# Performance work log

Hardware: AMD Instinct MI355X
Metric: run time of the kernel (lower is better)

Reference implementation:

```python
import jax, jax.numpy as jnp
import numpy as np

B, CN, DEG, IN_F, OUT_F, K = 32, 1024, 2, 128, 128, 10
NODES = [1, 16, 128, 1024]


def setup_inputs() -> dict:
    key = jax.random.key(0)
    ks = jax.random.split(key, 16)
    d = {}
    for i, n in enumerate(NODES):
        d[f"tree{i}"] = jax.random.normal(ks[i], (B, n, IN_F), dtype=jnp.float32)
    for i in range(4):
        d[f"Uw{i}"] = jax.random.normal(ks[4 + i], (IN_F, OUT_F), dtype=jnp.float32) * 0.05
        d[f"Ub{i}"] = jnp.zeros((OUT_F,), dtype=jnp.float32)
    d["W_up"] = jax.random.normal(ks[8], (CN, IN_F, DEG * IN_F), dtype=jnp.float32) * 0.05
    d["Fw0"] = jax.random.normal(ks[9], (IN_F, K * IN_F), dtype=jnp.float32) * 0.05
    d["Fb0"] = jnp.zeros((K * IN_F,), dtype=jnp.float32)
    d["Fw1"] = jax.random.normal(ks[10], (K * IN_F, OUT_F), dtype=jnp.float32) * 0.05
    d["Fb1"] = jnp.zeros((OUT_F,), dtype=jnp.float32)
    d["b_bias"] = jax.random.normal(ks[11], (1, DEG * CN, OUT_F), dtype=jnp.float32) * 0.05
    return d


def reference(tree0, tree1, tree2, tree3,
              Uw0, Ub0, Uw1, Ub1, Uw2, Ub2, Uw3, Ub3,
              W_up, Fw0, Fb0, Fw1, Fb1, b_bias):
    tree = [tree0, tree1, tree2, tree3]
    Uw = [Uw0, Uw1, Uw2, Uw3]
    Ub = [Ub0, Ub1, Ub2, Ub3]
    curr_node = W_up.shape[0]
    in_feat = W_up.shape[1]
    degree = W_up.shape[2] // in_feat

    # Ancestor info: project each depth, then tile each ancestor node's
    # projected vector to cover its descendants at the current level.
    anc = jnp.zeros((tree[0].shape[0], curr_node, Uw0.shape[1]), dtype=tree0.dtype)
    for t, w, b in zip(tree, Uw, Ub):
        Q = t @ w + b                       # [B, anc_node, out_feat]
        rep = curr_node // t.shape[1]
        anc = anc + jnp.repeat(Q, rep, axis=1)  # == tf.tile([1,1,rep]) + reshape

    # Per-node unique-weight upsample: [B,n,1,in] @ [n,in,deg*in]
    nl = jnp.einsum('bni,nio->bno', tree[-1], W_up)            # [B, CN, deg*in]
    nl = nl.reshape(nl.shape[0], curr_node * degree, in_feat)   # [B, CN*deg, in]
    nl = (nl @ Fw0 + Fb0) @ Fw1 + Fb1                           # Dense chain
    nl = nl + jnp.repeat(anc, degree, axis=1)                   # broadcast ancestors
    nl = nl + b_bias
    return jnp.where(nl >= 0, nl, 0.2 * nl)                     # LeakyReLU(0.2)
```

## Files before the change

kernel.cpp:

```cpp
#include <hip/hip_runtime.h>
#include <stdint.h>


using short8   = __attribute__((ext_vector_type(8))) short;
using floatx16 = __attribute__((ext_vector_type(16))) float;

__device__ __forceinline__ unsigned short f2bf(float f) {
    unsigned int u = __builtin_bit_cast(unsigned int, f);
    return (unsigned short)((u + 0x8000u) >> 16);
}

#define FB_OFF  524288
#define FF_OFF  524416
#define UW_OFF  532608

__global__ __launch_bounds__(256) void ffused_p1(
    const float* __restrict__ Fw0, const float* __restrict__ Fb0,
    const float* __restrict__ Fw1, float* __restrict__ P)
{
    const int kc = blockIdx.x;
    const int i  = blockIdx.y;
    const int j  = threadIdx.x & 127;
    const int il = threadIdx.x >> 7;
    const int k0 = kc * 160 + il * 80;
    const float* __restrict__ src = (i < 128) ? (Fw0 + (size_t)i * 1280) : Fb0;
    float acc = 0.f;
    #pragma unroll 8
    for (int kk = 0; kk < 80; ++kk)
        acc += src[k0 + kk] * Fw1[(size_t)(k0 + kk) * 128 + j];
    P[(size_t)(kc * 2 + il) * 16512 + i * 128 + j] = acc;
}

__global__ __launch_bounds__(256) void prep2(
    const float* __restrict__ P, const float* __restrict__ Fb1,
    const float* __restrict__ Uw0, const float* __restrict__ Uw1,
    const float* __restrict__ Uw2, const float* __restrict__ Uw3,
    unsigned short* __restrict__ FfusedBF, float* __restrict__ Fbias,
    unsigned short* __restrict__ UwBF)
{
    if (blockIdx.x < 65) {
        const int idx = blockIdx.x * 256 + threadIdx.x;
        if (idx >= 16512) return;
        const int i = idx >> 7, j = idx & 127;
        float s = 0.f;
        #pragma unroll
        for (int p = 0; p < 16; ++p) s += P[(size_t)p * 16512 + idx];
        if (i < 128) FfusedBF[(((i >> 3) * 128) + j) * 8 + (i & 7)] = f2bf(s);
        else         Fbias[j] = s + Fb1[j];
    } else {
        const int bx  = blockIdx.x - 65;
        const int mat = bx >> 4;
        const int kg  = bx & 15;
        const float* __restrict__ Uw = (mat == 0) ? Uw0 : (mat == 1) ? Uw1
                                     : (mat == 2) ? Uw2 : Uw3;
        const int col = threadIdx.x & 127;
        const int kh  = threadIdx.x >> 7;
        #pragma unroll
        for (int q = 0; q < 4; ++q) {
            const int kk = kh * 4 + q;
            const float v = Uw[(size_t)(kg * 8 + kk) * 128 + col];
            UwBF[(((size_t)(mat * 16 + kg) * 128) + col) * 8 + kk] = f2bf(v);
        }
    }
}

__global__ __launch_bounds__(256, 2) void tree_main(
    const float* __restrict__ t0, const float* __restrict__ t1,
    const float* __restrict__ t2, const float* __restrict__ t3,
    const float* __restrict__ Ub0, const float* __restrict__ Ub1,
    const float* __restrict__ Ub2, const float* __restrict__ Ub3,
    const float* __restrict__ Wup, const float* __restrict__ bbias,
    const unsigned short* __restrict__ FfusedBF,
    const unsigned short* __restrict__ UwBF,
    const float* __restrict__ Fbias,
    float* __restrict__ out)
{
    const int n    = blockIdx.x;
    const int tid  = threadIdx.x;
    const int w    = tid >> 6;
    const int lane = tid & 63;
    const int l31  = lane & 31;
    const int half = lane >> 5;
    const int colq = w * 32 + l31;
    const int i2   = n >> 3;

    __shared__ __align__(16) unsigned char smem_raw[33792 + 2 * 16384];
    unsigned short* Alds = (unsigned short*)smem_raw;
    unsigned short* Ulds = (unsigned short*)smem_raw;
    float* wbuf0 = (float*)(smem_raw + 33792);
    float* wbuf1 = (float*)(smem_raw + 33792 + 16384);

    const float* __restrict__ Wtile = Wup + (size_t)n * 32768;
#define ISSUE_W(T, WB) \
    { _Pragma("unroll") \
      for (int q = 0; q < 4; ++q) { \
        const int chunk = (tid >> 6) * 4 + q; \
        const float* gp = Wtile + (T) * 4096 + chunk * 256 + (tid & 63) * 4; \
        float* lp = (WB) + chunk * 256; \
        __builtin_amdgcn_global_load_lds( \
            (const __attribute__((address_space(1))) unsigned int*)gp, \
            (__attribute__((address_space(3))) unsigned int*)lp, 16, 0, 0); \
      } }

    ISSUE_W(0, wbuf0)
    ISSUE_W(1, wbuf1)

    #pragma unroll
    for (int mi = 0; mi < 4; ++mi) {
        const float* __restrict__ base = (mi == 0) ? t0 : (mi == 1) ? t1
                                       : (mi == 2) ? t2 : t3;
        #pragma unroll
        for (int i = 0; i < 4; ++i) {
            const int idx = i * 256 + tid;
            const int b   = idx >> 5;
            const int q   = idx & 31;
            int row;
            if      (mi == 0) row = b;
            else if (mi == 1) row = b * 16 + (i2 >> 3);
            else if (mi == 2) row = b * 128 + i2;
            else              row = b * 1024 + n;
            const float4 v = *reinterpret_cast<const float4*>(
                base + (size_t)row * 128 + q * 4);
            ushort4 u;
            u.x = f2bf(v.x); u.y = f2bf(v.y); u.z = f2bf(v.z); u.w = f2bf(v.w);
            *reinterpret_cast<ushort4*>(
                &Alds[((mi * 16 + (q >> 1)) * 33 + b) * 8 + (q & 1) * 4]) = u;
        }
    }
    __syncthreads();

    floatx16 qacc, accT0, accT1;
    #pragma unroll
    for (int r = 0; r < 16; ++r) { qacc[r] = 0.f; accT0[r] = 0.f; accT1[r] = 0.f; }

    #pragma unroll
    for (int ks = 0; ks < 24; ++ks) {
        const int kg = 2 * ks + half;
        const short8 a  = *reinterpret_cast<const short8*>(&Alds[(kg * 33 + l31) * 8]);
        const short8 bf = *reinterpret_cast<const short8*>(
            &UwBF[((size_t)kg * 128 + colq) * 8]);
        qacc = __builtin_amdgcn_mfma_f32_32x32x16_bf16(a, bf, qacc, 0, 0, 0);
    }

#define WBODY_L(WT, WB) \
    { const int kg = 48 + 2 * (WT) + half; \
      const short8 a  = *reinterpret_cast<const short8*>(&Alds[(kg * 33 + l31) * 8]); \
      const short8 bf = *reinterpret_cast<const short8*>( \
          &UwBF[((size_t)kg * 128 + colq) * 8]); \
      qacc = __builtin_amdgcn_mfma_f32_32x32x16_bf16(a, bf, qacc, 0, 0, 0); \
      short8 a0, a1; \
      _Pragma("unroll") \
      for (int jj = 0; jj < 8; ++jj) { \
          a0[jj] = (short)f2bf((WB)[(half * 8 + jj) * 256 + w * 64 + l31]); \
          a1[jj] = (short)f2bf((WB)[(half * 8 + jj) * 256 + w * 64 + 32 + l31]); } \
      accT0 = __builtin_amdgcn_mfma_f32_32x32x16_bf16(a0, a, accT0, 0, 0, 0); \
      accT1 = __builtin_amdgcn_mfma_f32_32x32x16_bf16(a1, a, accT1, 0, 0, 0); }

    WBODY_L(0, wbuf0) __syncthreads(); ISSUE_W(2, wbuf0)
    WBODY_L(1, wbuf1) __syncthreads(); ISSUE_W(3, wbuf1)
    WBODY_L(2, wbuf0) __syncthreads(); ISSUE_W(4, wbuf0)
    WBODY_L(3, wbuf1) __syncthreads(); ISSUE_W(5, wbuf1)
    WBODY_L(4, wbuf0) __syncthreads(); ISSUE_W(6, wbuf0)
    WBODY_L(5, wbuf1) __syncthreads(); ISSUE_W(7, wbuf1)
    WBODY_L(6, wbuf0) __syncthreads();
    WBODY_L(7, wbuf1)

    __syncthreads();

    #pragma unroll
    for (int tt = 0; tt < 2; ++tt) {
        const floatx16 Av = tt ? accT1 : accT0;
        #pragma unroll
        for (int r = 0; r < 16; ++r) {
            const int cm = w * 64 + tt * 32 + ((r & 3) + 8 * (r >> 2) + 4 * half);
            const int d  = cm >> 7;
            const int cp = cm & 127;
            Ulds[(((cp >> 3) * 65) + d * 32 + l31) * 8 + (cp & 7)] = f2bf(Av[r]);
        }
    }
    __syncthreads();

    const float ubsum = Ub0[colq] + Ub1[colq] + Ub2[colq] + Ub3[colq] + Fbias[colq];
    const float bb0 = bbias[(size_t)(2 * n + 0) * 128 + colq];
    const float bb1 = bbias[(size_t)(2 * n + 1) * 128 + colq];

    floatx16 o0, o1;
    #pragma unroll
    for (int r = 0; r < 16; ++r) { o0[r] = 0.f; o1[r] = 0.f; }
    #pragma unroll
    for (int ks = 0; ks < 8; ++ks) {
        const int kg2 = 2 * ks + half;
        const short8 a0 = *reinterpret_cast<const short8*>(&Ulds[(kg2 * 65 + l31) * 8]);
        const short8 a1 = *reinterpret_cast<const short8*>(&Ulds[(kg2 * 65 + 32 + l31) * 8]);
        const short8 bf = *reinterpret_cast<const short8*>(
            &FfusedBF[(((size_t)kg2 * 128) + colq) * 8]);
        o0 = __builtin_amdgcn_mfma_f32_32x32x16_bf16(a0, bf, o0, 0, 0, 0);
        o1 = __builtin_amdgcn_mfma_f32_32x32x16_bf16(a1, bf, o1, 0, 0, 0);
    }

    #pragma unroll
    for (int r = 0; r < 16; ++r) {
        const int brow = (r & 3) + 8 * (r >> 2) + 4 * half;
        const float addc = qacc[r] + ubsum;
        float v0 = o0[r] + addc + bb0;
        float v1 = o1[r] + addc + bb1;
        v0 = (v0 >= 0.f) ? v0 : 0.2f * v0;
        v1 = (v1 >= 0.f) ? v1 : 0.2f * v1;
        const size_t idx0 = ((size_t)brow * 2048 + 2 * n) * 128 + colq;
        out[idx0]       = v0;
        out[idx0 + 128] = v1;
    }
}

extern "C" void kernel_launch(void* const* d_in, const int* in_sizes, int n_in,
                              void* d_out, int out_size, void* d_ws, size_t ws_size,
                              hipStream_t stream) {
    const float* t0  = (const float*)d_in[0];
    const float* t1  = (const float*)d_in[1];
    const float* t2  = (const float*)d_in[2];
    const float* t3  = (const float*)d_in[3];
    const float* Uw0 = (const float*)d_in[4];
    const float* Ub0 = (const float*)d_in[5];
    const float* Uw1 = (const float*)d_in[6];
    const float* Ub1 = (const float*)d_in[7];
    const float* Uw2 = (const float*)d_in[8];
    const float* Ub2 = (const float*)d_in[9];
    const float* Uw3 = (const float*)d_in[10];
    const float* Ub3 = (const float*)d_in[11];
    const float* Wup = (const float*)d_in[12];
    const float* Fw0 = (const float*)d_in[13];
    const float* Fb0 = (const float*)d_in[14];
    const float* Fw1 = (const float*)d_in[15];
    const float* Fb1 = (const float*)d_in[16];
    const float* bb  = (const float*)d_in[17];

    float* ws = (float*)d_ws;
    float* P              = ws;
    float* Fbias          = ws + FB_OFF;
    unsigned short* FfBF  = (unsigned short*)(ws + FF_OFF);
    unsigned short* UwBF  = (unsigned short*)(ws + UW_OFF);

    ffused_p1<<<dim3(8, 129), 256, 0, stream>>>(Fw0, Fb0, Fw1, P);
    prep2<<<129, 256, 0, stream>>>(P, Fb1, Uw0, Uw1, Uw2, Uw3, FfBF, Fbias, UwBF);
    tree_main<<<1024, 256, 0, stream>>>(t0, t1, t2, t3,
                                        Ub0, Ub1, Ub2, Ub3,
                                        Wup, bb, FfBF, UwBF,
                                        Fbias, (float*)d_out);
}
```

Baseline: 263.8 us.

## Stage full W_up tile in LDS up front and swizzle A layout

Replaces the two-buffer W_up streaming pipeline with a single up-front load of all eight 16 KB W_up tiles into a 128 KB LDS region. This removes the per-tile barriers in the main loop. The padded A layout is replaced by an XOR swizzle to avoid LDS bank conflicts without padding. Launch bounds drop to one block per CU because of the larger LDS footprint, which reduces latency hiding across blocks. All W loads now complete before compute starts, so load and compute no longer overlap within a block.

```diff
diff --git a/kernel.cpp b/kernel.cpp
--- a/kernel.cpp
+++ b/kernel.cpp
@@ -64,7 +64,9 @@
     }
 }
 
-__global__ __launch_bounds__(256, 2) void tree_main(
+#define AIDX(KG, B) ((((KG) * 32) + ((B) ^ ((KG) & 7))) * 8)
+
+__global__ __launch_bounds__(256, 1) void tree_main(
     const float* __restrict__ t0, const float* __restrict__ t1,
     const float* __restrict__ t2, const float* __restrict__ t3,
     const float* __restrict__ Ub0, const float* __restrict__ Ub1,
@@ -84,26 +86,25 @@
     const int colq = w * 32 + l31;
     const int i2   = n >> 3;
 
-    __shared__ __align__(16) unsigned char smem_raw[33792 + 2 * 16384];
+    __shared__ __align__(16) unsigned char smem_raw[32768 + 131072];
     unsigned short* Alds = (unsigned short*)smem_raw;
     unsigned short* Ulds = (unsigned short*)smem_raw;
-    float* wbuf0 = (float*)(smem_raw + 33792);
-    float* wbuf1 = (float*)(smem_raw + 33792 + 16384);
+    float* wlds = (float*)(smem_raw + 32768);
 
     const float* __restrict__ Wtile = Wup + (size_t)n * 32768;
-#define ISSUE_W(T, WB) \
+#define ISSUE_W(T) \
     { _Pragma("unroll") \
       for (int q = 0; q < 4; ++q) { \
         const int chunk = (tid >> 6) * 4 + q; \
         const float* gp = Wtile + (T) * 4096 + chunk * 256 + (tid & 63) * 4; \
-        float* lp = (WB) + chunk * 256; \
+        float* lp = wlds + (T) * 4096 + chunk * 256; \
         __builtin_amdgcn_global_load_lds( \
             (const __attribute__((address_space(1))) unsigned int*)gp, \
             (__attribute__((address_space(3))) unsigned int*)lp, 16, 0, 0); \
       } }
 
-    ISSUE_W(0, wbuf0)
-    ISSUE_W(1, wbuf1)
+    ISSUE_W(0) ISSUE_W(1) ISSUE_W(2) ISSUE_W(3)
+    ISSUE_W(4) ISSUE_W(5) ISSUE_W(6) ISSUE_W(7)
 
     #pragma unroll
     for (int mi = 0; mi < 4; ++mi) {
@@ -123,8 +124,8 @@
                 base + (size_t)row * 128 + q * 4);
             ushort4 u;
             u.x = f2bf(v.x); u.y = f2bf(v.y); u.z = f2bf(v.z); u.w = f2bf(v.w);
-            *reinterpret_cast<ushort4*>(
-                &Alds[((mi * 16 + (q >> 1)) * 33 + b) * 8 + (q & 1) * 4]) = u;
+            const int kg = mi * 16 + (q >> 1);
+            *reinterpret_cast<ushort4*>(&Alds[AIDX(kg, b) + (q & 1) * 4]) = u;
         }
     }
     __syncthreads();
@@ -136,34 +137,29 @@
     #pragma unroll
     for (int ks = 0; ks < 24; ++ks) {
         const int kg = 2 * ks + half;
-        const short8 a  = *reinterpret_cast<const short8*>(&Alds[(kg * 33 + l31) * 8]);
+        const short8 a  = *reinterpret_cast<const short8*>(&Alds[AIDX(kg, l31)]);
         const short8 bf = *reinterpret_cast<const short8*>(
             &UwBF[((size_t)kg * 128 + colq) * 8]);
         qacc = __builtin_amdgcn_mfma_f32_32x32x16_bf16(a, bf, qacc, 0, 0, 0);
     }
 
-#define WBODY_L(WT, WB) \
+#define WBODY_L(WT) \
     { const int kg = 48 + 2 * (WT) + half; \
-      const short8 a  = *reinterpret_cast<const short8*>(&Alds[(kg * 33 + l31) * 8]); \
+      const short8 a  = *reinterpret_cast<const short8*>(&Alds[AIDX(kg, l31)]); \
       const short8 bf = *reinterpret_cast<const short8*>( \
           &UwBF[((size_t)kg * 128 + colq) * 8]); \
       qacc = __builtin_amdgcn_mfma_f32_32x32x16_bf16(a, bf, qacc, 0, 0, 0); \
+      const float* __restrict__ WB = wlds + (WT) * 4096; \
       short8 a0, a1; \
       _Pragma("unroll") \
       for (int jj = 0; jj < 8; ++jj) { \
-          a0[jj] = (short)f2bf((WB)[(half * 8 + jj) * 256 + w * 64 + l31]); \
-          a1[jj] = (short)f2bf((WB)[(half * 8 + jj) * 256 + w * 64 + 32 + l31]); } \
+          a0[jj] = (short)f2bf(WB[(half * 8 + jj) * 256 + w * 64 + l31]); \
+          a1[jj] = (short)f2bf(WB[(half * 8 + jj) * 256 + w * 64 + 32 + l31]); } \
       accT0 = __builtin_amdgcn_mfma_f32_32x32x16_bf16(a0, a, accT0, 0, 0, 0); \
       accT1 = __builtin_amdgcn_mfma_f32_32x32x16_bf16(a1, a, accT1, 0, 0, 0); }
 
-    WBODY_L(0, wbuf0) __syncthreads(); ISSUE_W(2, wbuf0)
-    WBODY_L(1, wbuf1) __syncthreads(); ISSUE_W(3, wbuf1)
-    WBODY_L(2, wbuf0) __syncthreads(); ISSUE_W(4, wbuf0)
-    WBODY_L(3, wbuf1) __syncthreads(); ISSUE_W(5, wbuf1)
-    WBODY_L(4, wbuf0) __syncthreads(); ISSUE_W(6, wbuf0)
-    WBODY_L(5, wbuf1) __syncthreads(); ISSUE_W(7, wbuf1)
-    WBODY_L(6, wbuf0) __syncthreads();
-    WBODY_L(7, wbuf1)
+    WBODY_L(0) WBODY_L(1) WBODY_L(2) WBODY_L(3)
+    WBODY_L(4) WBODY_L(5) WBODY_L(6) WBODY_L(7)
 
     __syncthreads();
 
```

Measured after the change: 280.1 us. 1.06x slower.
